# Kernel tuning notes

Hardware: AMD Instinct MI355X
Metric: run time of the kernel (lower is better)

## Reference

```python
import jax, jax.numpy as jnp
import numpy as np

NUM_GRAPHS = 512
N_NODES = 131072
N_EDGES = 4194304
F_IN = 54
H_GCN = 16
H_LSTM = 32
N_CLASSES = 192
MAX_SEQ_LEN = 1024


def setup_inputs() -> dict:
    key = jax.random.key(0)
    ks = jax.random.split(key, 12)
    s = 0.1
    return {
        "x": jax.random.normal(ks[0], (N_NODES, F_IN), jnp.float32),
        "edge_index": jax.random.randint(ks[1], (2, N_EDGES), 0, N_NODES),
        "batch": jnp.sort(jax.random.randint(ks[2], (N_NODES,), 0, NUM_GRAPHS)),
        "gcn_w1": jax.random.normal(ks[3], (F_IN, H_GCN), jnp.float32) * s,
        "gcn_b1": jnp.zeros((H_GCN,), jnp.float32),
        "gcn_w2": jax.random.normal(ks[4], (H_GCN, H_GCN), jnp.float32) * s,
        "gcn_b2": jnp.zeros((H_GCN,), jnp.float32),
        "lstm0_wih": jax.random.normal(ks[5], (2, 4 * H_LSTM, H_GCN), jnp.float32) * s,
        "lstm0_whh": jax.random.normal(ks[6], (2, 4 * H_LSTM, H_LSTM), jnp.float32) * s,
        "lstm0_bih": jnp.zeros((2, 4 * H_LSTM), jnp.float32),
        "lstm0_bhh": jnp.zeros((2, 4 * H_LSTM), jnp.float32),
        "lstm1_wih": jax.random.normal(ks[7], (2, 4 * H_LSTM, 2 * H_LSTM), jnp.float32) * s,
        "lstm1_whh": jax.random.normal(ks[8], (2, 4 * H_LSTM, H_LSTM), jnp.float32) * s,
        "lstm1_bih": jnp.zeros((2, 4 * H_LSTM), jnp.float32),
        "lstm1_bhh": jnp.zeros((2, 4 * H_LSTM), jnp.float32),
        "fc_w": jax.random.normal(ks[9], (2 * H_LSTM, N_CLASSES), jnp.float32) * s,
        "fc_b": jnp.zeros((N_CLASSES,), jnp.float32),
        "max_seq_len": MAX_SEQ_LEN,
    }


def _lstm_dir(xseq, wih, whh, bih, bhh, reverse):
    # xseq: [B, T, D]; PyTorch gate order i, f, g, o.
    pre = jnp.einsum("btd,gd->btg", xseq, wih) + bih + bhh  # [B, T, 4H]
    B = xseq.shape[0]
    H = whh.shape[-1]

    def step(carry, g_t):
        h, c = carry
        g = g_t + h @ whh.T
        i, f, gg, o = jnp.split(g, 4, axis=-1)
        c = jax.nn.sigmoid(f) * c + jax.nn.sigmoid(i) * jnp.tanh(gg)
        h = jax.nn.sigmoid(o) * jnp.tanh(c)
        return (h, c), h

    init = (jnp.zeros((B, H), xseq.dtype), jnp.zeros((B, H), xseq.dtype))
    _, hs = jax.lax.scan(step, init, jnp.swapaxes(pre, 0, 1), reverse=reverse)
    return jnp.swapaxes(hs, 0, 1)  # [B, T, H]


def _bilstm(xseq, wih, whh, bih, bhh):
    fwd = _lstm_dir(xseq, wih[0], whh[0], bih[0], bhh[0], reverse=False)
    bwd = _lstm_dir(xseq, wih[1], whh[1], bih[1], bhh[1], reverse=True)
    return jnp.concatenate([fwd, bwd], axis=-1)


def reference(x, edge_index, batch, gcn_w1, gcn_b1, gcn_w2, gcn_b2,
              lstm0_wih, lstm0_whh, lstm0_bih, lstm0_bhh,
              lstm1_wih, lstm1_whh, lstm1_bih, lstm1_bhh,
              fc_w, fc_b, max_seq_len):
    N = x.shape[0]
    loop = jnp.arange(N)
    src = jnp.concatenate([edge_index[0], loop])  # GCNConv adds self-loops
    dst = jnp.concatenate([edge_index[1], loop])
    deg = jax.ops.segment_sum(jnp.ones_like(dst, jnp.float32), dst, num_segments=N)
    dinv = jax.lax.rsqrt(jnp.maximum(deg, 1.0))  # deg >= 1 due to self-loops
    norm = (dinv[src] * dinv[dst])[:, None]

    def conv(h, W, b):
        msg = (h @ W)[src] * norm
        return jax.ops.segment_sum(msg, dst, num_segments=N) + b

    h = jax.nn.relu(conv(x, gcn_w1, gcn_b1))
    # F.dropout(training=False) is identity in eval mode
    h = jax.nn.relu(conv(h, gcn_w2, gcn_b2))

    # Ragged -> padded [NUM_GRAPHS, max_seq_len, H_GCN] (batch is graph-sorted)
    counts = jax.ops.segment_sum(jnp.ones((N,), jnp.int32), batch, num_segments=NUM_GRAPHS)
    starts = jnp.concatenate([jnp.zeros((1,), jnp.int32), jnp.cumsum(counts)[:-1]])
    pos = jnp.arange(N) - starts[batch]
    padded = jnp.zeros((NUM_GRAPHS, max_seq_len, h.shape[1]), h.dtype).at[batch, pos].set(h, mode="drop")

    seq = _bilstm(padded, lstm0_wih, lstm0_whh, lstm0_bih, lstm0_bhh)
    seq = _bilstm(seq, lstm1_wih, lstm1_whh, lstm1_bih, lstm1_bhh)
    pooled = jnp.mean(seq, axis=1)  # mean over padded length, as in original
    return pooled @ fc_w + fc_b
```

## Files before the change

kernel.cpp:

```cpp
#include <hip/hip_runtime.h>
#include <cstdint>
#include <cstddef>

#define NG 512
#define NN 131072
#define NE 4194304
#define FIN 54
#define HG 16
#define HL 32
#define NC 192
#define TS 1024

#define NB 256
#define WH 512
#define EPW (NE/WH)

__device__ __forceinline__ float rcpf(float x){ return __builtin_amdgcn_rcpf(x); }
__device__ __forceinline__ float sigf(float x){ return rcpf(1.0f + __expf(-x)); }
__device__ __forceinline__ float tanhfast(float x){ return 1.0f - 2.0f*rcpf(__expf(2.0f*x) + 1.0f); }

__device__ __forceinline__ float4 uload4(const float* p){
  unsigned long long a = (unsigned long long)p;
  asm volatile("" : "+v"(a));
  return *(const float4*)a;
}

#define CEPS 1e-6f
#define HEPS 1e-6f

__global__ void k_initc(int* __restrict__ counts){
  counts[threadIdx.x] = 0;
}

__global__ void k_cnt(const int* __restrict__ batch, int* __restrict__ counts){
  int i = blockIdx.x*256 + threadIdx.x;
  if (i < NN) atomicAdd(&counts[batch[i]], 1);
}

__global__ void k_scan(const int* __restrict__ counts, int* __restrict__ starts){
  __shared__ int sc[NG];
  int t = threadIdx.x;
  sc[t] = counts[t]; __syncthreads();
  for (int off = 1; off < NG; off <<= 1){
    int v = (t >= off) ? sc[t-off] : 0;
    __syncthreads();
    sc[t] += v;
    __syncthreads();
  }
  starts[t] = sc[t] - counts[t];
}

__global__ void k_hist(const int* __restrict__ ei, int* __restrict__ hist){
  int w = blockIdx.x, tid = threadIdx.x;
  __shared__ int h[NB];
  h[tid] = 0;
  __syncthreads();
  int e0 = w*EPW;
  for (int i = tid; i < EPW; i += 256) atomicAdd(&h[ei[NE + e0 + i] >> 9], 1);
  __syncthreads();
  hist[tid*WH + w] = h[tid];
}

__global__ void k_scanH(const int* __restrict__ hist, int* __restrict__ offs,
                        int* __restrict__ bstart){
  __shared__ int tot[1024];
  int t = threadIdx.x;
  int base = t*128;
  int s = 0;
  for (int i = 0; i < 128; i++) s += hist[base + i];
  tot[t] = s; __syncthreads();
  for (int o = 1; o < 1024; o <<= 1){
    int v = (t >= o) ? tot[t-o] : 0;
    __syncthreads();
    tot[t] += v;
    __syncthreads();
  }
  int run = tot[t] - s;
  for (int i = 0; i < 128; i++){
    int idx = base + i;
    int h = hist[idx];
    offs[idx] = run;
    if ((idx & (WH-1)) == 0) bstart[idx / WH] = run;
    run += h;
  }
  if (t == 0) bstart[NB] = NE;
}

__global__ void k_binB(const int* __restrict__ ei, const int* __restrict__ offs,
                       uint2* __restrict__ pair){
  int w = blockIdx.x, tid = threadIdx.x;
  __shared__ int cur[NB];
  cur[tid] = offs[tid*WH + w];
  __syncthreads();
  int e0 = w*EPW;
  for (int i = tid; i < EPW; i += 256){
    int e = e0 + i;
    int s = ei[e], d = ei[NE + e];
    int b = d >> 9;
    int pos = atomicAdd(&cur[b], 1);
    pair[pos] = make_uint2((unsigned)s, (unsigned)(d & 511));
  }
}

__global__ void k_binC(const uint2* __restrict__ pair, const int* __restrict__ bstart,
                       int* __restrict__ eoff, int* __restrict__ ecnt, int* __restrict__ csr){
  int b = blockIdx.x, tid = threadIdx.x;
  __shared__ int h2[512];
  __shared__ int cur[512];
  h2[tid] = 0; h2[tid + 256] = 0;
  __syncthreads();
  int e0 = bstart[b], e1 = bstart[b+1];
  for (int i = e0 + tid; i < e1; i += 256) atomicAdd(&h2[pair[i].y], 1);
  __syncthreads();
  cur[tid] = h2[tid]; cur[tid + 256] = h2[tid + 256];
  __syncthreads();
  for (int o = 1; o < 256; o <<= 1){
    int v0 = (tid >= o) ? cur[tid - o] : 0;
    int v1 = (tid >= o) ? cur[256 + tid - o] : 0;
    __syncthreads();
    cur[tid] += v0; cur[256 + tid] += v1;
    __syncthreads();
  }
  int half0 = cur[255];
  __syncthreads();
  cur[256 + tid] += half0;
  __syncthreads();
  int n0 = tid, n1 = tid + 256;
  int ex0 = cur[n0] - h2[n0];
  int ex1 = cur[n1] - h2[n1];
  eoff[b*512 + n0] = e0 + ex0; ecnt[b*512 + n0] = h2[n0];
  eoff[b*512 + n1] = e0 + ex1; ecnt[b*512 + n1] = h2[n1];
  __syncthreads();
  cur[n0] = e0 + ex0; cur[n1] = e0 + ex1;
  __syncthreads();
  for (int i = e0 + tid; i < e1; i += 256){
    uint2 u = pair[i];
    int pos = atomicAdd(&cur[u.y], 1);
    csr[pos] = (int)u.x;
  }
}

__global__ void k_dinv(const int* __restrict__ ecnt, float* __restrict__ dinv){
  int i = blockIdx.x*256 + threadIdx.x;
  if (i < NN) dinv[i] = 1.0f / sqrtf((float)(ecnt[i] + 1));
}

__global__ void k_lin1(const float* __restrict__ x, const float* __restrict__ w1,
                       float* __restrict__ xa){
  __shared__ float w[FIN*HG];
  __shared__ float xs[16][FIN+2];
  int tid = threadIdx.x;
  for (int i = tid; i < FIN*HG; i += 256) w[i] = w1[i];
  const float4* gx = (const float4*)(x + (size_t)blockIdx.x*16*FIN);
  if (tid < 216){
    float4 v4 = gx[tid];
    int fi = tid*4;
#pragma unroll
    for (int e = 0; e < 4; e++){
      int idx = fi + e;
      xs[idx/FIN][idx%FIN] = ((const float*)&v4)[e];
    }
  }
  __syncthreads();
  int node = tid >> 4, f = tid & 15;
  const float* xr = xs[node];
  float acc = 0.0f;
#pragma unroll
  for (int k = 0; k < FIN; k++) acc = fmaf(xr[k], w[k*HG + f], acc);
  xa[((size_t)blockIdx.x*16 + node)*HG + f] = acc;
}

__global__ void k_gather(const float* __restrict__ v, const int* __restrict__ csr,
                         const int* __restrict__ eoff, const int* __restrict__ ecnt,
                         const float* __restrict__ dinv, const float* __restrict__ bias,
                         int dorelu, float* __restrict__ out){
  int gid = blockIdx.x*16 + (threadIdx.x >> 4);
  int f = threadIdx.x & 15;
  float dv = dinv[gid];
  float a0 = v[(size_t)gid*HG + f] * dv, a1 = 0.0f, a2 = 0.0f, a3 = 0.0f;
  int o = eoff[gid], n = ecnt[gid];
  int i = 0;
  for (; i + 8 <= n; i += 8){
    int s0 = csr[o+i],   s1 = csr[o+i+1], s2 = csr[o+i+2], s3 = csr[o+i+3];
    int s4 = csr[o+i+4], s5 = csr[o+i+5], s6 = csr[o+i+6], s7 = csr[o+i+7];
    a0 = fmaf(v[(size_t)s0*HG + f], dinv[s0], a0);
    a1 = fmaf(v[(size_t)s1*HG + f], dinv[s1], a1);
    a2 = fmaf(v[(size_t)s2*HG + f], dinv[s2], a2);
    a3 = fmaf(v[(size_t)s3*HG + f], dinv[s3], a3);
    a0 = fmaf(v[(size_t)s4*HG + f], dinv[s4], a0);
    a1 = fmaf(v[(size_t)s5*HG + f], dinv[s5], a1);
    a2 = fmaf(v[(size_t)s6*HG + f], dinv[s6], a2);
    a3 = fmaf(v[(size_t)s7*HG + f], dinv[s7], a3);
  }
  for (; i + 4 <= n; i += 4){
    int s0 = csr[o+i], s1 = csr[o+i+1], s2 = csr[o+i+2], s3 = csr[o+i+3];
    a0 = fmaf(v[(size_t)s0*HG + f], dinv[s0], a0);
    a1 = fmaf(v[(size_t)s1*HG + f], dinv[s1], a1);
    a2 = fmaf(v[(size_t)s2*HG + f], dinv[s2], a2);
    a3 = fmaf(v[(size_t)s3*HG + f], dinv[s3], a3);
  }
  for (; i < n; i++){
    int s = csr[o+i];
    a0 = fmaf(v[(size_t)s*HG + f], dinv[s], a0);
  }
  float acc = ((a0 + a1) + (a2 + a3)) * dv;
  if (dorelu) acc = fmaxf(acc + bias[f], 0.0f);
  out[(size_t)gid*HG + f] = acc;
}

__global__ void k_relu_lin(const float* __restrict__ agg, const float* __restrict__ b1,
                           const float* __restrict__ w2, float* __restrict__ hb){
  __shared__ float w[HG*HG];
  __shared__ float bb[HG];
  int tid = threadIdx.x;
  if (tid < HG*HG) w[tid] = w2[tid];
  if (tid < HG) bb[tid] = b1[tid];
  __syncthreads();
  int id = blockIdx.x*256 + tid;
  if (id >= NN*HG) return;
  int node = id >> 4, f = id & 15;
  const float* ar = agg + (size_t)node*HG;
  float acc = 0.0f;
#pragma unroll
  for (int k = 0; k < HG; k++){
    float h = fmaxf(ar[k] + bb[k], 0.0f);
    acc = fmaf(h, w[k*HG + f], acc);
  }
  hb[id] = acc;
}


#define LTAIL() \
  float uA = (a0 + a1) + (a2 + a3); \
  float uB = (b0 + b1) + (b2 + b3); \
  float aA = sigf(uA); \
  float ub2 = half ? uB : (uB + uB); \
  float sv = sigf(ub2); \
  float aB = half ? sv : (sv + sv - 1.0f); \
  float pq = aA*aB; \
  float part = __shfl_xor(half ? aA : pq, 32); \
  float f_ = half ? aA : part; \
  float p_ = half ? part : pq; \
  float cn = fmaf(f_, c, p_); \
  float th = tanhfast(cn); \
  float ov = __shfl_xor(aB, 32); \
  float o_ = half ? aB : ov; \
  float hn = o_ * th;

__global__ __launch_bounds__(64, 1) void k_lstm0(
    const float* __restrict__ h2in, const int* __restrict__ starts, const int* __restrict__ counts,
    const float* __restrict__ wih, const float* __restrict__ whh,
    const float* __restrict__ bih, const float* __restrict__ bhh,
    float* __restrict__ out0, int* __restrict__ tconv, int* __restrict__ az)
{
  const int g = blockIdx.x >> 1, dir = blockIdx.x & 1;
  const int lane = threadIdx.x;
  const int j = lane & 31, half = lane >> 5;
  const int rA = (half ? 32 : 0) + j;
  const int rB = rA + 64;
  float wxA[HG], wxB[HG], whA[HL], whB[HL];
  { const float4* a4 = (const float4*)(wih + ((size_t)dir*128 + rA)*HG);
    const float4* b4 = (const float4*)(wih + ((size_t)dir*128 + rB)*HG);
#pragma unroll
    for (int k = 0; k < HG/4; k++){ ((float4*)wxA)[k] = a4[k]; ((float4*)wxB)[k] = b4[k]; }
    const float4* ua4 = (const float4*)(whh + ((size_t)dir*128 + rA)*HL);
    const float4* ub4 = (const float4*)(whh + ((size_t)dir*128 + rB)*HL);
#pragma unroll
    for (int k = 0; k < HL/4; k++){ ((float4*)whA)[k] = ua4[k]; ((float4*)whB)[k] = ub4[k]; }
  }
  const float pbA = bih[dir*128 + rA] + bhh[dir*128 + rA];
  const float pbB = bih[dir*128 + rB] + bhh[dir*128 + rB];
  int cnt = counts[g]; if (cnt > TS) cnt = TS;
  const int s0 = starts[g];
  float* outg = out0 + (size_t)g*TS*64 + dir*32;

  __shared__ __align__(16) float hbuf[HL];

  unsigned long long bz = __ballot((pbA == 0.0f) && (pbB == 0.0f));
  bool allzero = (bz == ~0ull);
  if (dir == 1 && lane == 0) az[0] = allzero ? 1 : 0;
  if (!half) hbuf[j] = 0.0f;
  float4 H[8];
  { const float4* h4r = (const float4*)hbuf;
#pragma unroll
    for (int q = 0; q < 8; q++) H[q] = h4r[q]; }

  float c = 0.0f, h = 0.0f;
  int t, dt, tendF;

#define L0_HFMA() \
  _Pragma("unroll") \
  for (int q = 0; q < 8; q++){ float4 hq = H[q]; \
    a0 = fmaf(hq.x, whA[4*q+0], a0); a1 = fmaf(hq.y, whA[4*q+1], a1); \
    a2 = fmaf(hq.z, whA[4*q+2], a2); a3 = fmaf(hq.w, whA[4*q+3], a3); \
    b0 = fmaf(hq.x, whB[4*q+0], b0); b1 = fmaf(hq.y, whB[4*q+1], b1); \
    b2 = fmaf(hq.z, whB[4*q+2], b2); b3 = fmaf(hq.w, whB[4*q+3], b3); }

#define L0_STORE() \
  c = cn; h = hn; \
  if (!half) hbuf[j] = h; \
  { const float4* h4r = (const float4*)hbuf; \
    _Pragma("unroll") for (int q = 0; q < 8; q++) H[q] = h4r[q]; } \
  if (half) outg[(size_t)t*64 + j] = h;

#define L0_F(P) { \
  if (t == tendF) goto l0_fdone; \
  float a0 = pbA, a1 = 0.0f, a2 = 0.0f, a3 = 0.0f; \
  float b0 = pbB, b1 = 0.0f, b2 = 0.0f, b3 = 0.0f; \
  _Pragma("unroll") \
  for (int q = 0; q < 4; q++){ float4 xq = XR##P[q]; \
    a0 = fmaf(xq.x, wxA[4*q+0], a0); a1 = fmaf(xq.y, wxA[4*q+1], a1); \
    a2 = fmaf(xq.z, wxA[4*q+2], a2); a3 = fmaf(xq.w, wxA[4*q+3], a3); \
    b0 = fmaf(xq.x, wxB[4*q+0], b0); b1 = fmaf(xq.y, wxB[4*q+1], b1); \
    b2 = fmaf(xq.z, wxB[4*q+2], b2); b3 = fmaf(xq.w, wxB[4*q+3], b3); } \
  { int tp = t + 4*dt; tp = tp < 0 ? 0 : (tp > cnt-1 ? cnt-1 : tp); \
    const float* pp = h2in + (size_t)(s0 + tp)*HG; \
    XR##P[0] = uload4(pp); XR##P[1] = uload4(pp+4); \
    XR##P[2] = uload4(pp+8); XR##P[3] = uload4(pp+12); } \
  L0_HFMA(); \
  LTAIL(); \
  L0_STORE(); \
  t += dt; }

  if (dir == 1 && !allzero){
    for (t = TS - 1; t >= cnt; t--){
      float a0 = pbA, a1 = 0.0f, a2 = 0.0f, a3 = 0.0f;
      float b0 = pbB, b1 = 0.0f, b2 = 0.0f, b3 = 0.0f;
      L0_HFMA();
      LTAIL();
      L0_STORE();
    }
  }

  if (cnt > 0){
    if (dir == 0){ t = 0; dt = 1; tendF = cnt; }
    else { t = cnt - 1; dt = -1; tendF = -1; }
    if (!(dir == 1 && t < 0)){
      float4 XR0[4], XR1[4], XR2[4], XR3[4];
      { int r1 = t + dt, r2 = t + 2*dt, r3 = t + 3*dt;
        r1 = r1 < 0 ? 0 : (r1 > cnt-1 ? cnt-1 : r1);
        r2 = r2 < 0 ? 0 : (r2 > cnt-1 ? cnt-1 : r2);
        r3 = r3 < 0 ? 0 : (r3 > cnt-1 ? cnt-1 : r3);
        const float* p0 = h2in + (size_t)(s0 + t)*HG;
        const float* p1 = h2in + (size_t)(s0 + r1)*HG;
        const float* p2 = h2in + (size_t)(s0 + r2)*HG;
        const float* p3 = h2in + (size_t)(s0 + r3)*HG;
        XR0[0]=uload4(p0); XR0[1]=uload4(p0+4); XR0[2]=uload4(p0+8); XR0[3]=uload4(p0+12);
        XR1[0]=uload4(p1); XR1[1]=uload4(p1+4); XR1[2]=uload4(p1+8); XR1[3]=uload4(p1+12);
        XR2[0]=uload4(p2); XR2[1]=uload4(p2+4); XR2[2]=uload4(p2+8); XR2[3]=uload4(p2+12);
        XR3[0]=uload4(p3); XR3[1]=uload4(p3+4); XR3[2]=uload4(p3+8); XR3[3]=uload4(p3+12);
      }
      for (;;){ L0_F(0); L0_F(1); L0_F(2); L0_F(3); }
l0_fdone: ;
    }
  }

  if (dir == 0){
    bool fwdconv = false;
    for (t = cnt; t < TS; t++){
      float a0 = pbA, a1 = 0.0f, a2 = 0.0f, a3 = 0.0f;
      float b0 = pbB, b1 = 0.0f, b2 = 0.0f, b3 = 0.0f;
      L0_HFMA();
      LTAIL();
      bool eq = (fabsf(cn - c) <= CEPS*(1.0f + fabsf(cn))) && (fabsf(hn - h) <= HEPS);
      L0_STORE();
      unsigned long long m = __ballot(eq);
      if (t >= cnt + 1 && m == ~0ull){
        if (lane == 0) tconv[g] = t - 1;
        fwdconv = true;
        break;
      }
    }
    if (!fwdconv && lane == 0) tconv[g] = TS;
  }
#undef L0_F
#undef L0_STORE
#undef L0_HFMA
}

__global__ __launch_bounds__(64, 1) void k_lstm1(
    const float* __restrict__ gl0, const int* __restrict__ tconv,
    const int* __restrict__ counts, const int* __restrict__ az,
    const float* __restrict__ wih, const float* __restrict__ whh,
    const float* __restrict__ bih, const float* __restrict__ bhh,
    float* __restrict__ pooled)
{
  const int g = blockIdx.x >> 1, dir = blockIdx.x & 1;
  const int lane = threadIdx.x;
  const int j = lane & 31, half = lane >> 5;
  const int rA = (half ? 32 : 0) + j, rB = rA + 64;
  float wxA[64], wxB[64], whA[HL], whB[HL];
  { const float4* A4 = (const float4*)(wih + ((size_t)dir*128 + rA)*64);
    const float4* B4 = (const float4*)(wih + ((size_t)dir*128 + rB)*64);
#pragma unroll
    for (int k = 0; k < 16; k++){ ((float4*)wxA)[k] = A4[k]; ((float4*)wxB)[k] = B4[k]; }
    const float4* a4 = (const float4*)(whh + ((size_t)dir*128 + rA)*HL);
    const float4* b4 = (const float4*)(whh + ((size_t)dir*128 + rB)*HL);
#pragma unroll
    for (int k = 0; k < 8; k++){ ((float4*)whA)[k] = a4[k]; ((float4*)whB)[k] = b4[k]; }
  }
  const float pbA = bih[dir*128 + rA] + bhh[dir*128 + rA];
  const float pbB = bih[dir*128 + rB] + bhh[dir*128 + rB];
  const float* gin = gl0 + (size_t)g*TS*64;
  const int tcv = tconv[g];
  int cnt = counts[g]; if (cnt > TS) cnt = TS;
  const bool mz = (az[0] != 0) && (half != 0);

  __shared__ __align__(16) float hbuf[HL];
  __shared__ __align__(16) float xrow[2][64];

  if (!half) hbuf[j] = 0.0f;

  float c = 0.0f, h = 0.0f, hsum = 0.0f;
  float xA0, xA1, xA2, xA3, xB0, xB1, xB2, xB3;
  float v1, v2, v3;
  int t;

#define L1_MASKV(TN, V) ((mz && (TN) >= cnt) ? 0.0f : (V))

#define L1_GATES8(N0,N1,N2,N3,M0,M1,M2,M3, XP) \
  N0 = pbA; N1 = 0.0f; N2 = 0.0f; N3 = 0.0f; \
  M0 = pbB; M1 = 0.0f; M2 = 0.0f; M3 = 0.0f; \
  { const float4* xp_ = (const float4*)(XP); \
    _Pragma("unroll") \
    for (int q = 0; q < 16; q++){ float4 xq = xp_[q]; \
      N0 = fmaf(xq.x, wxA[4*q+0], N0); N1 = fmaf(xq.y, wxA[4*q+1], N1); \
      N2 = fmaf(xq.z, wxA[4*q+2], N2); N3 = fmaf(xq.w, wxA[4*q+3], N3); \
      M0 = fmaf(xq.x, wxB[4*q+0], M0); M1 = fmaf(xq.y, wxB[4*q+1], M1); \
      M2 = fmaf(xq.z, wxB[4*q+2], M2); M3 = fmaf(xq.w, wxB[4*q+3], M3); } }

#define L1_HFMA8(A0,A1,A2,A3,B0,B1,B2,B3) \
  { const float4* h4_ = (const float4*)hbuf; \
    _Pragma("unroll") \
    for (int q = 0; q < 8; q++){ float4 hq = h4_[q]; \
      A0 = fmaf(hq.x, whA[4*q+0], A0); A1 = fmaf(hq.y, whA[4*q+1], A1); \
      A2 = fmaf(hq.z, whA[4*q+2], A2); A3 = fmaf(hq.w, whA[4*q+3], A3); \
      B0 = fmaf(hq.x, whB[4*q+0], B0); B1 = fmaf(hq.y, whB[4*q+1], B1); \
      B2 = fmaf(hq.z, whB[4*q+2], B2); B3 = fmaf(hq.w, whB[4*q+3], B3); } }

#define L1_PSTEP(DT) { \
  L1_HFMA8(xA0,xA1,xA2,xA3,xB0,xB1,xB2,xB3); \
  float uA = (xA0 + xA1) + (xA2 + xA3); \
  float uB = (xB0 + xB1) + (xB2 + xB3); \
  float actA = sigf(uA); \
  float ub2 = half ? uB : (uB + uB); \
  float sv = sigf(ub2); \
  float actB = half ? sv : (sv + sv - 1.0f); \
  float pq_ = actA*actB; \
  float part = __shfl_xor(half ? actA : pq_, 32); \
  float n0,n1,n2,n3,m0,m1,m2,m3; \
  L1_GATES8(n0,n1,n2,n3,m0,m1,m2,m3, xrow[(t+1)&1]); \
  { int tn = t + 2*(DT); int tnc = tn < 0 ? 0 : (tn > TS-1 ? TS-1 : tn); \
    xrow[t&1][lane] = L1_MASKV(tnc, v1); } \
  v1 = v2; v2 = v3; \
  { int tp = t + 5*(DT); tp = tp < 0 ? 0 : (tp > TS-1 ? TS-1 : tp); \
    v3 = gin[(size_t)tp*64 + lane]; } \
  float f_ = half ? actA : part; \
  float p_ = half ? part : pq_; \
  float cn = fmaf(f_, c, p_); \
  float th = tanhfast(cn); \
  c = cn; \
  if (half){ float hn = actB * th; h = hn; hbuf[j] = hn; hsum += hn; } \
  xA0=n0; xA1=n1; xA2=n2; xA3=n3; xB0=m0; xB1=m1; xB2=m2; xB3=m3; }

#define L1_CSTEP(EQ) \
  float a0 = xA0, a1 = xA1, a2 = xA2, a3 = xA3; \
  float b0 = xB0, b1 = xB1, b2 = xB2, b3 = xB3; \
  L1_HFMA8(a0,a1,a2,a3,b0,b1,b2,b3); \
  float uA = (a0 + a1) + (a2 + a3); \
  float uB = (b0 + b1) + (b2 + b3); \
  float actA = sigf(uA); \
  float ub2 = half ? uB : (uB + uB); \
  float sv = sigf(ub2); \
  float actB = half ? sv : (sv + sv - 1.0f); \
  float pq_ = actA*actB; \
  float part = __shfl_xor(half ? actA : pq_, 32); \
  float f_ = half ? actA : part; \
  float p_ = half ? part : pq_; \
  float cn = fmaf(f_, c, p_); \
  float th = tanhfast(cn); \
  float hn = actB * th; \
  bool EQ = (fabsf(cn - c) <= CEPS*(1.0f + fabsf(cn))) && (!half || (fabsf(hn - h) <= HEPS)); \
  c = cn; \
  if (half){ h = hn; hbuf[j] = hn; hsum += hn; }

  if (dir == 0){
    const int tend = (tcv < TS-1) ? tcv : TS-1;
    xrow[0][lane] = L1_MASKV(0, gin[lane]);
    { int r = 1; xrow[1][lane] = L1_MASKV(r, gin[(size_t)r*64 + lane]); }
    v1 = gin[(size_t)2*64 + lane];
    v2 = gin[(size_t)3*64 + lane];
    v3 = gin[(size_t)4*64 + lane];
    L1_GATES8(xA0,xA1,xA2,xA3,xB0,xB1,xB2,xB3, xrow[0]);
    for (t = 0; t <= tend; t++) L1_PSTEP(1);
    if (tcv < TS-1){
      for (int tt = tcv+1; tt < TS; tt++){
        L1_CSTEP(eq);
        unsigned long long m = __ballot(eq);
        if (m == ~0ull){ hsum += h * (float)(TS-1 - tt); break; }
      }
    }
  } else {
    int tfull;
    if (tcv + 1 <= TS - 1){
      { int r = tcv+1;
        xrow[0][lane] = L1_MASKV(r, gin[(size_t)r*64 + lane]); }
      L1_GATES8(xA0,xA1,xA2,xA3,xB0,xB1,xB2,xB3, xrow[0]);
      int tt = TS - 1; bool jumped = false;
      for (; tt >= tcv + 1; tt--){
        L1_CSTEP(eq);
        unsigned long long m = __ballot(eq);
        if (m == ~0ull){ hsum += h * (float)(tt - tcv); jumped = true; break; }
      }
      tfull = jumped ? (tcv - 1) : tcv;
    } else tfull = TS - 1;
    if (tfull >= 0){
      { int r = tfull;
        xrow[r&1][lane] = L1_MASKV(r, gin[(size_t)r*64 + lane]); }
      { int r = tfull-1; int rc = r < 0 ? 0 : r;
        xrow[(tfull+1)&1][lane] = L1_MASKV(rc, gin[(size_t)rc*64 + lane]); }
      { int r = tfull-2; if (r < 0) r = 0; v1 = gin[(size_t)r*64 + lane]; }
      { int r = tfull-3; if (r < 0) r = 0; v2 = gin[(size_t)r*64 + lane]; }
      { int r = tfull-4; if (r < 0) r = 0; v3 = gin[(size_t)r*64 + lane]; }
      L1_GATES8(xA0,xA1,xA2,xA3,xB0,xB1,xB2,xB3, xrow[tfull&1]);
      for (t = tfull; t >= 0; t--) L1_PSTEP(-1);
    }
  }
  if (half) pooled[(size_t)g*64 + dir*32 + j] = hsum * (1.0f/(float)TS);
#undef L1_MASKV
#undef L1_GATES8
#undef L1_HFMA8
#undef L1_PSTEP
#undef L1_CSTEP
}

__global__ void k_fc(const float* __restrict__ pooled, const float* __restrict__ fcw,
                     const float* __restrict__ fcb, float* __restrict__ out){
  __shared__ float p[64];
  int g = blockIdx.x, cix = threadIdx.x;
  if (cix < 64) p[cix] = pooled[(size_t)g*64 + cix];
  __syncthreads();
  float acc = fcb[cix];
#pragma unroll
  for (int k = 0; k < 64; k++) acc = fmaf(p[k], fcw[k*NC + cix], acc);
  out[(size_t)g*NC + cix] = acc;
}

extern "C" void kernel_launch(void* const* d_in, const int* in_sizes, int n_in,
                              void* d_out, int out_size, void* d_ws, size_t ws_size,
                              hipStream_t stream) {
  const float* x        = (const float*)d_in[0];
  const int*   ei       = (const int*)  d_in[1];
  const int*   batch    = (const int*)  d_in[2];
  const float* gcn_w1   = (const float*)d_in[3];
  const float* gcn_b1   = (const float*)d_in[4];
  const float* gcn_w2   = (const float*)d_in[5];
  const float* gcn_b2   = (const float*)d_in[6];
  const float* l0_wih   = (const float*)d_in[7];
  const float* l0_whh   = (const float*)d_in[8];
  const float* l0_bih   = (const float*)d_in[9];
  const float* l0_bhh   = (const float*)d_in[10];
  const float* l1_wih   = (const float*)d_in[11];
  const float* l1_whh   = (const float*)d_in[12];
  const float* l1_bih   = (const float*)d_in[13];
  const float* l1_bhh   = (const float*)d_in[14];
  const float* fc_w     = (const float*)d_in[15];
  const float* fc_b     = (const float*)d_in[16];
  float* out = (float*)d_out;

  float* ws   = (float*)d_ws;
  float* B0   = ws;
  float* B1   = B0 + (size_t)NN*HG;
  float* B2   = B1 + (size_t)NN*HG;
  float* dinv = B2 + (size_t)NN*HG;
  int*   ecnt   = (int*)(dinv + NN);
  int*   eoff   = ecnt + NN;
  int*   hist   = eoff + NN;
  int*   offs   = hist + NB*WH;
  int*   counts = offs + NB*WH;
  int*   starts = counts + NG;
  int*   tconv  = starts + NG;
  int*   bstart = tconv + NG;
  int*   az     = bstart + NB + 4;
  float* pooled = (float*)(bstart + NB + 64);
  int*   csr    = (int*)(pooled + (size_t)NG*64);
  float* out0   = (float*)(csr + (size_t)NE);
  uint2* pair   = (uint2*)out0;
  size_t needed = ((size_t)((float*)out0 - ws) + (size_t)NG*TS*64) * sizeof(float);
  if (ws_size < needed) return;

  k_initc <<<1, NG, 0, stream>>>(counts);
  k_cnt   <<<NN/256, 256, 0, stream>>>(batch, counts);
  k_hist  <<<WH, 256, 0, stream>>>(ei, hist);
  k_scanH <<<1, 1024, 0, stream>>>(hist, offs, bstart);
  k_scan  <<<1, NG, 0, stream>>>(counts, starts);
  k_binB  <<<WH, 256, 0, stream>>>(ei, offs, pair);
  k_binC  <<<NB, 256, 0, stream>>>(pair, bstart, eoff, ecnt, csr);
  k_dinv  <<<NN/256, 256, 0, stream>>>(ecnt, dinv);
  k_lin1  <<<NN/16, 256, 0, stream>>>(x, gcn_w1, B0);
  k_gather<<<(NN*HG)/256, 256, 0, stream>>>(B0, csr, eoff, ecnt, dinv, gcn_b2, 0, B1);
  k_relu_lin<<<(NN*HG)/256, 256, 0, stream>>>(B1, gcn_b1, gcn_w2, B2);
  k_gather<<<(NN*HG)/256, 256, 0, stream>>>(B2, csr, eoff, ecnt, dinv, gcn_b2, 1, B1);
  k_lstm0 <<<NG*2, 64, 0, stream>>>(B1, starts, counts, l0_wih, l0_whh, l0_bih, l0_bhh, out0, tconv, az);
  k_lstm1 <<<NG*2, 64, 0, stream>>>(out0, tconv, counts, az, l1_wih, l1_whh, l1_bih, l1_bhh, pooled);
  k_fc    <<<NG, NC, 0, stream>>>(pooled, fc_w, fc_b, out);
}
```

Measured before the change: 953.3 us.

## Split LSTM1 into producer/consumer wavefronts with shared-memory ring buffer

```diff
diff --git a/kernel.cpp b/kernel.cpp
--- a/kernel.cpp
+++ b/kernel.cpp
@@ -378,7 +378,7 @@
 #undef L0_HFMA
 }
 
-__global__ __launch_bounds__(64, 1) void k_lstm1(
+__global__ __launch_bounds__(128, 1) void k_lstm1(
     const float* __restrict__ gl0, const int* __restrict__ tconv,
     const int* __restrict__ counts, const int* __restrict__ az,
     const float* __restrict__ wih, const float* __restrict__ whh,
@@ -386,50 +386,103 @@
     float* __restrict__ pooled)
 {
   const int g = blockIdx.x >> 1, dir = blockIdx.x & 1;
-  const int lane = threadIdx.x;
+  const int tid = threadIdx.x;
+  const int wid = tid >> 6;
+  const int lane = tid & 63;
   const int j = lane & 31, half = lane >> 5;
   const int rA = (half ? 32 : 0) + j, rB = rA + 64;
-  float wxA[64], wxB[64], whA[HL], whB[HL];
-  { const float4* A4 = (const float4*)(wih + ((size_t)dir*128 + rA)*64);
-    const float4* B4 = (const float4*)(wih + ((size_t)dir*128 + rB)*64);
-#pragma unroll
-    for (int k = 0; k < 16; k++){ ((float4*)wxA)[k] = A4[k]; ((float4*)wxB)[k] = B4[k]; }
-    const float4* a4 = (const float4*)(whh + ((size_t)dir*128 + rA)*HL);
-    const float4* b4 = (const float4*)(whh + ((size_t)dir*128 + rB)*HL);
-#pragma unroll
-    for (int k = 0; k < 8; k++){ ((float4*)whA)[k] = a4[k]; ((float4*)whB)[k] = b4[k]; }
-  }
-  const float pbA = bih[dir*128 + rA] + bhh[dir*128 + rA];
-  const float pbB = bih[dir*128 + rB] + bhh[dir*128 + rB];
+
   const float* gin = gl0 + (size_t)g*TS*64;
   const int tcv = tconv[g];
   int cnt = counts[g]; if (cnt > TS) cnt = TS;
-  const bool mz = (az[0] != 0) && (half != 0);
-
+  const bool spec = (tcv + 1 <= TS - 1);
+  const int K = spec ? (tcv + 2) : TS;
+
+  __shared__ __align__(16) float ring[8*16*64];
+  __shared__ int fl[16];
+  __shared__ int nsh;
+  __shared__ __align__(16) float xrow[2][64];
   __shared__ __align__(16) float hbuf[HL];
-  __shared__ __align__(16) float xrow[2][64];
-
-  if (!half) hbuf[j] = 0.0f;
-
-  float c = 0.0f, h = 0.0f, hsum = 0.0f;
-  float xA0, xA1, xA2, xA3, xB0, xB1, xB2, xB3;
-  float v1, v2, v3;
-  int t;
-
-#define L1_MASKV(TN, V) ((mz && (TN) >= cnt) ? 0.0f : (V))
-
-#define L1_GATES8(N0,N1,N2,N3,M0,M1,M2,M3, XP) \
-  N0 = pbA; N1 = 0.0f; N2 = 0.0f; N3 = 0.0f; \
-  M0 = pbB; M1 = 0.0f; M2 = 0.0f; M3 = 0.0f; \
-  { const float4* xp_ = (const float4*)(XP); \
-    _Pragma("unroll") \
-    for (int q = 0; q < 16; q++){ float4 xq = xp_[q]; \
-      N0 = fmaf(xq.x, wxA[4*q+0], N0); N1 = fmaf(xq.y, wxA[4*q+1], N1); \
-      N2 = fmaf(xq.z, wxA[4*q+2], N2); N3 = fmaf(xq.w, wxA[4*q+3], N3); \
-      M0 = fmaf(xq.x, wxB[4*q+0], M0); M1 = fmaf(xq.y, wxB[4*q+1], M1); \
-      M2 = fmaf(xq.z, wxB[4*q+2], M2); M3 = fmaf(xq.w, wxB[4*q+3], M3); } }
-
-#define L1_HFMA8(A0,A1,A2,A3,B0,B1,B2,B3) \
+
+  if (tid < 16) fl[tid] = -1;
+  if (tid == 16) nsh = 0;
+  if (wid == 1 && !half) hbuf[j] = 0.0f;
+  __syncthreads();
+
+  volatile int* nv = (volatile int*)&nsh;
+
+  if (wid == 0){
+    const bool mzp = (az[0] != 0) && (half != 0);
+    float wxA[64], wxB[64];
+    { const float4* A4 = (const float4*)(wih + ((size_t)dir*128 + rA)*64);
+      const float4* B4 = (const float4*)(wih + ((size_t)dir*128 + rB)*64);
+#pragma unroll
+      for (int k = 0; k < 16; k++){ ((float4*)wxA)[k] = A4[k]; ((float4*)wxB)[k] = B4[k]; }
+    }
+    const float pbA = bih[dir*128 + rA] + bhh[dir*128 + rA];
+    const float pbB = bih[dir*128 + rB] + bhh[dir*128 + rB];
+
+#define P_ROW(KK) (dir == 0 ? (KK) : (spec ? ((KK) == 0 ? tcv+1 : tcv+1-(KK)) : TS-1-(KK)))
+#define P_ROWCL(KK) P_ROW((KK) < 0 ? 0 : ((KK) > K-1 ? K-1 : (KK)))
+
+    { int r0 = P_ROW(0);
+      float xv = gin[(size_t)r0*64 + lane];
+      if (mzp && r0 >= cnt) xv = 0.0f;
+      xrow[0][lane] = xv; }
+    float v1 = gin[(size_t)P_ROWCL(1)*64 + lane];
+    float v2 = gin[(size_t)P_ROWCL(2)*64 + lane];
+    float v3 = gin[(size_t)P_ROWCL(3)*64 + lane];
+
+    for (int k = 0; k < K; k++){
+      int r = P_ROW(k);
+      while (*nv < k - 15) __builtin_amdgcn_s_sleep(2);
+      float a0 = pbA, a1 = 0.0f, a2 = 0.0f, a3 = 0.0f;
+      float b0 = pbB, b1 = 0.0f, b2 = 0.0f, b3 = 0.0f;
+      { const float4* xp_ = (const float4*)xrow[k & 1];
+#pragma unroll
+        for (int q = 0; q < 16; q++){ float4 xq = xp_[q];
+          a0 = fmaf(xq.x, wxA[4*q+0], a0); a1 = fmaf(xq.y, wxA[4*q+1], a1);
+          a2 = fmaf(xq.z, wxA[4*q+2], a2); a3 = fmaf(xq.w, wxA[4*q+3], a3);
+          b0 = fmaf(xq.x, wxB[4*q+0], b0); b1 = fmaf(xq.y, wxB[4*q+1], b1);
+          b2 = fmaf(xq.z, wxB[4*q+2], b2); b3 = fmaf(xq.w, wxB[4*q+3], b3); } }
+      if (k + 1 < K){
+        int rn = P_ROW(k+1);
+        float xw = (mzp && rn >= cnt) ? 0.0f : v1;
+        xrow[(k+1) & 1][lane] = xw;
+        v1 = v2; v2 = v3;
+        v3 = gin[(size_t)P_ROWCL(k+4)*64 + lane];
+      }
+      int slot = r & 15;
+      float* rp = ring + slot*64 + lane;
+      rp[0]    = a0; rp[1024] = a1; rp[2048] = a2; rp[3072] = a3;
+      rp[4096] = b0; rp[5120] = b1; rp[6144] = b2; rp[7168] = b3;
+      asm volatile("s_waitcnt lgkmcnt(0)" ::: "memory");
+      *(volatile int*)&fl[slot] = r;
+    }
+#undef P_ROW
+#undef P_ROWCL
+  } else {
+    float whA[HL], whB[HL];
+    { const float4* a4 = (const float4*)(whh + ((size_t)dir*128 + rA)*HL);
+      const float4* b4 = (const float4*)(whh + ((size_t)dir*128 + rB)*HL);
+#pragma unroll
+      for (int k = 0; k < 8; k++){ ((float4*)whA)[k] = a4[k]; ((float4*)whB)[k] = b4[k]; }
+    }
+    float c = 0.0f, h = 0.0f, hsum = 0.0f;
+    float xA0, xA1, xA2, xA3, xB0, xB1, xB2, xB3;
+    int ncount = 0;
+
+#define C_SPINREAD(T) { int t_ = (T), slot_ = t_ & 15; \
+  volatile int* fp_ = (volatile int*)&fl[slot_]; \
+  while (*fp_ != t_) {} \
+  asm volatile("" ::: "memory"); \
+  const float* rp_ = ring + slot_*64 + lane; \
+  xA0 = rp_[0];    xA1 = rp_[1024]; xA2 = rp_[2048]; xA3 = rp_[3072]; \
+  xB0 = rp_[4096]; xB1 = rp_[5120]; xB2 = rp_[6144]; xB3 = rp_[7168]; }
+
+#define C_PUB() { ncount++; if (lane == 0) *nv = ncount; }
+
+#define C_HFMA8(A0,A1,A2,A3,B0,B1,B2,B3) \
   { const float4* h4_ = (const float4*)hbuf; \
     _Pragma("unroll") \
     for (int q = 0; q < 8; q++){ float4 hq = h4_[q]; \
@@ -438,35 +491,29 @@
       B0 = fmaf(hq.x, whB[4*q+0], B0); B1 = fmaf(hq.y, whB[4*q+1], B1); \
       B2 = fmaf(hq.z, whB[4*q+2], B2); B3 = fmaf(hq.w, whB[4*q+3], B3); } }
 
-#define L1_PSTEP(DT) { \
-  L1_HFMA8(xA0,xA1,xA2,xA3,xB0,xB1,xB2,xB3); \
-  float uA = (xA0 + xA1) + (xA2 + xA3); \
-  float uB = (xB0 + xB1) + (xB2 + xB3); \
+#define C_STEP() { \
+  float a0 = xA0, a1 = xA1, a2 = xA2, a3 = xA3; \
+  float b0 = xB0, b1 = xB1, b2 = xB2, b3 = xB3; \
+  C_HFMA8(a0,a1,a2,a3,b0,b1,b2,b3); \
+  float uA = (a0 + a1) + (a2 + a3); \
+  float uB = (b0 + b1) + (b2 + b3); \
   float actA = sigf(uA); \
   float ub2 = half ? uB : (uB + uB); \
   float sv = sigf(ub2); \
   float actB = half ? sv : (sv + sv - 1.0f); \
   float pq_ = actA*actB; \
   float part = __shfl_xor(half ? actA : pq_, 32); \
-  float n0,n1,n2,n3,m0,m1,m2,m3; \
-  L1_GATES8(n0,n1,n2,n3,m0,m1,m2,m3, xrow[(t+1)&1]); \
-  { int tn = t + 2*(DT); int tnc = tn < 0 ? 0 : (tn > TS-1 ? TS-1 : tn); \
-    xrow[t&1][lane] = L1_MASKV(tnc, v1); } \
-  v1 = v2; v2 = v3; \
-  { int tp = t + 5*(DT); tp = tp < 0 ? 0 : (tp > TS-1 ? TS-1 : tp); \
-    v3 = gin[(size_t)tp*64 + lane]; } \
   float f_ = half ? actA : part; \
   float p_ = half ? part : pq_; \
   float cn = fmaf(f_, c, p_); \
   float th = tanhfast(cn); \
   c = cn; \
-  if (half){ float hn = actB * th; h = hn; hbuf[j] = hn; hsum += hn; } \
-  xA0=n0; xA1=n1; xA2=n2; xA3=n3; xB0=m0; xB1=m1; xB2=m2; xB3=m3; }
-
-#define L1_CSTEP(EQ) \
+  if (half){ float hn = actB * th; h = hn; hbuf[j] = hn; hsum += hn; } }
+
+#define C_CSTEP(EQ) \
   float a0 = xA0, a1 = xA1, a2 = xA2, a3 = xA3; \
   float b0 = xB0, b1 = xB1, b2 = xB2, b3 = xB3; \
-  L1_HFMA8(a0,a1,a2,a3,b0,b1,b2,b3); \
+  C_HFMA8(a0,a1,a2,a3,b0,b1,b2,b3); \
   float uA = (a0 + a1) + (a2 + a3); \
   float uB = (b0 + b1) + (b2 + b3); \
   float actA = sigf(uA); \
@@ -484,54 +531,42 @@
   c = cn; \
   if (half){ h = hn; hbuf[j] = hn; hsum += hn; }
 
-  if (dir == 0){
-    const int tend = (tcv < TS-1) ? tcv : TS-1;
-    xrow[0][lane] = L1_MASKV(0, gin[lane]);
-    { int r = 1; xrow[1][lane] = L1_MASKV(r, gin[(size_t)r*64 + lane]); }
-    v1 = gin[(size_t)2*64 + lane];
-    v2 = gin[(size_t)3*64 + lane];
-    v3 = gin[(size_t)4*64 + lane];
-    L1_GATES8(xA0,xA1,xA2,xA3,xB0,xB1,xB2,xB3, xrow[0]);
-    for (t = 0; t <= tend; t++) L1_PSTEP(1);
-    if (tcv < TS-1){
-      for (int tt = tcv+1; tt < TS; tt++){
-        L1_CSTEP(eq);
-        unsigned long long m = __ballot(eq);
-        if (m == ~0ull){ hsum += h * (float)(TS-1 - tt); break; }
+    if (dir == 0){
+      const int tend = (tcv < TS-1) ? tcv : TS-1;
+      for (int t = 0; t <= tend; t++){
+        C_SPINREAD(t); C_STEP(); C_PUB();
       }
-    }
-  } else {
-    int tfull;
-    if (tcv + 1 <= TS - 1){
-      { int r = tcv+1;
-        xrow[0][lane] = L1_MASKV(r, gin[(size_t)r*64 + lane]); }
-      L1_GATES8(xA0,xA1,xA2,xA3,xB0,xB1,xB2,xB3, xrow[0]);
-      int tt = TS - 1; bool jumped = false;
-      for (; tt >= tcv + 1; tt--){
-        L1_CSTEP(eq);
-        unsigned long long m = __ballot(eq);
-        if (m == ~0ull){ hsum += h * (float)(tt - tcv); jumped = true; break; }
+      if (spec){
+        C_SPINREAD(tcv+1); C_PUB();
+        for (int tt = tcv+1; tt < TS; tt++){
+          C_CSTEP(eq);
+          unsigned long long m = __ballot(eq);
+          if (m == ~0ull){ hsum += h * (float)(TS-1 - tt); break; }
+        }
       }
-      tfull = jumped ? (tcv - 1) : tcv;
-    } else tfull = TS - 1;
-    if (tfull >= 0){
-      { int r = tfull;
-        xrow[r&1][lane] = L1_MASKV(r, gin[(size_t)r*64 + lane]); }
-      { int r = tfull-1; int rc = r < 0 ? 0 : r;
-        xrow[(tfull+1)&1][lane] = L1_MASKV(rc, gin[(size_t)rc*64 + lane]); }
-      { int r = tfull-2; if (r < 0) r = 0; v1 = gin[(size_t)r*64 + lane]; }
-      { int r = tfull-3; if (r < 0) r = 0; v2 = gin[(size_t)r*64 + lane]; }
-      { int r = tfull-4; if (r < 0) r = 0; v3 = gin[(size_t)r*64 + lane]; }
-      L1_GATES8(xA0,xA1,xA2,xA3,xB0,xB1,xB2,xB3, xrow[tfull&1]);
-      for (t = tfull; t >= 0; t--) L1_PSTEP(-1);
-    }
-  }
-  if (half) pooled[(size_t)g*64 + dir*32 + j] = hsum * (1.0f/(float)TS);
-#undef L1_MASKV
-#undef L1_GATES8
-#undef L1_HFMA8
-#undef L1_PSTEP
-#undef L1_CSTEP
+    } else {
+      int tfull;
+      if (spec){
+        C_SPINREAD(tcv+1); C_PUB();
+        bool jumped = false;
+        for (int tt = TS-1; tt >= tcv+1; tt--){
+          C_CSTEP(eq);
+          unsigned long long m = __ballot(eq);
+          if (m == ~0ull){ hsum += h * (float)(tt - tcv); jumped = true; break; }
+        }
+        tfull = jumped ? (tcv - 1) : tcv;
+      } else tfull = TS - 1;
+      for (int t = tfull; t >= 0; t--){
+        C_SPINREAD(t); C_STEP(); C_PUB();
+      }
+    }
+    if (half) pooled[(size_t)g*64 + dir*32 + j] = hsum * (1.0f/(float)TS);
+#undef C_SPINREAD
+#undef C_PUB
+#undef C_HFMA8
+#undef C_STEP
+#undef C_CSTEP
+  }
 }
 
 __global__ void k_fc(const float* __restrict__ pooled, const float* __restrict__ fcw,
@@ -602,6 +637,6 @@
   k_relu_lin<<<(NN*HG)/256, 256, 0, stream>>>(B1, gcn_b1, gcn_w2, B2);
   k_gather<<<(NN*HG)/256, 256, 0, stream>>>(B2, csr, eoff, ecnt, dinv, gcn_b2, 1, B1);
   k_lstm0 <<<NG*2, 64, 0, stream>>>(B1, starts, counts, l0_wih, l0_whh, l0_bih, l0_bhh, out0, tconv, az);
-  k_lstm1 <<<NG*2, 64, 0, stream>>>(out0, tconv, counts, az, l1_wih, l1_whh, l1_bih, l1_bhh, pooled);
+  k_lstm1 <<<NG*2, 128, 0, stream>>>(out0, tconv, counts, az, l1_wih, l1_whh, l1_bih, l1_bhh, pooled);
   k_fc    <<<NG, NC, 0, stream>>>(pooled, fc_w, fc_b, out);
 }
```

Measured after the change: 995.1 us. 4.4% more time.
